# Optimization experiments

Hardware: AMD Instinct MI355X
Metric: run time of the kernel (lower is better)

## Reference

```python
import jax, jax.numpy as jnp
import numpy as np

B, S, IN, H, L = 512, 1024, 64, 32, 4


def setup_inputs() -> dict:
    key = jax.random.key(0)
    ks = jax.random.split(key, 9)
    s = 1.0 / np.sqrt(H)  # PyTorch RNN/Linear init scale
    u = lambda k, shape: jax.random.uniform(k, shape, jnp.float32, -s, s)
    return {
        "x": jax.random.normal(ks[0], (B, S, IN), jnp.float32),
        "h_state": jnp.zeros((L, B, H), jnp.float32),
        "W_ih0": u(ks[1], (H, IN)),          # layer 0 input weights
        "W_ih_rest": u(ks[2], (L - 1, H, H)),  # layers 1..3 input weights
        "W_hh": u(ks[3], (L, H, H)),
        "b_ih": u(ks[4], (L, H)),
        "b_hh": u(ks[5], (L, H)),
        "fc_w": u(ks[6], (1, H)),
        "fc_b": u(ks[7], (1,)),
    }


def _rnn_layer(seq_sbf, h0, W_ih, W_hh, b):
    # seq_sbf: [S, B, F]; vanilla RNN: h_t = tanh(x_t W_ih^T + h_{t-1} W_hh^T + b)
    def step(h, x_t):
        h = jnp.tanh(x_t @ W_ih.T + h @ W_hh.T + b)
        return h, h
    return jax.lax.scan(step, h0, seq_sbf)


def reference(x, h_state, W_ih0, W_ih_rest, W_hh, b_ih, b_hh, fc_w, fc_b):
    seq = jnp.swapaxes(x, 0, 1)  # [S, B, IN]
    h_finals = []
    for l in range(L):  # fixed small layer count
        W_ih = W_ih0 if l == 0 else W_ih_rest[l - 1]
        h_last, seq = _rnn_layer(seq, h_state[l], W_ih, W_hh[l], b_ih[l] + b_hh[l])
        h_finals.append(h_last)
    r_out = jnp.swapaxes(seq, 0, 1)                 # [B, S, H]
    logits = (r_out @ fc_w.T + fc_b)[..., 0]        # fused per-timestep Linear -> [B, S]
    probs = jax.nn.softmax(logits, axis=-1)         # nn.Softmax over last (seq) dim
    return probs, jnp.stack(h_finals, axis=0)       # [B,S], [L,B,H]
```

## Files before the change

### kernel.cpp

```cpp
#include <hip/hip_runtime.h>


#define BB 512
#define SS 1024
#define INF 64
#define HH 32
#define LL 4
#define KB 16

typedef __fp16 v2h __attribute__((ext_vector_type(2)));

__device__ __forceinline__ v2h bch(unsigned u) { return __builtin_bit_cast(v2h, u); }
__device__ __forceinline__ unsigned bcu(v2h h) { return __builtin_bit_cast(unsigned, h); }

template <int CTRL>
__device__ __forceinline__ float dpp_add(float v) {
  int y = __builtin_amdgcn_update_dpp(0, __float_as_int(v), CTRL, 0xF, 0xF, true);
  return v + __int_as_float(y);
}
template <int CTRL>
__device__ __forceinline__ float dpp_mov(float v) {
  int y = __builtin_amdgcn_update_dpp(0, __float_as_int(v), CTRL, 0xF, 0xF, true);
  return __int_as_float(y);
}

__device__ __forceinline__ float tanh_fast(float a) {
  const float e = __builtin_amdgcn_exp2f(a * 2.885390081777927f);
  const float r = __builtin_amdgcn_rcpf(e + 1.0f);
  return __builtin_fmaf(-2.0f, r, 1.0f);
}

__device__ __forceinline__ float dot16p(const v2h* w, const v2h* v) {
  float a = 0.f, c = 0.f;
#pragma unroll
  for (int j = 0; j < 4; ++j) {
    a = __builtin_amdgcn_fdot2(w[2 * j + 0], v[2 * j + 0], a, false);
    c = __builtin_amdgcn_fdot2(w[2 * j + 1], v[2 * j + 1], c, false);
  }
  return a + c;
}

#define BAR() asm volatile("s_waitcnt lgkmcnt(0)\n\ts_barrier" ::: "memory")

__global__ __launch_bounds__(512, 4) void rnn_kernel(
    const float* __restrict__ x, const float* __restrict__ h_state,
    const float* __restrict__ W_ih0, const float* __restrict__ W_ih_rest,
    const float* __restrict__ W_hh, const float* __restrict__ b_ih,
    const float* __restrict__ b_hh, const float* __restrict__ fc_w,
    const float* __restrict__ fc_b, float* __restrict__ out) {
  __shared__ int hb[LL][2][KB][16];
  __shared__ float h3f[2][KB][32];
  __shared__ float lu0[2][KB][32];
  __shared__ float lrow[SS];
  __shared__ float red[8];

  const int tid  = threadIdx.x;
  const int wid  = tid >> 6;
  const int lane = tid & 63;
  const int b    = blockIdx.x;
  const int ks   = lane & 1;
  const int h    = lane >> 1;

  v2h wih[8], whh[8];
  float bias = 0.f;
  if (wid < LL) {
    const float2* ph = (const float2*)(W_hh + (size_t)(wid * HH + h) * HH + ks * 16);
#pragma unroll
    for (int j = 0; j < 8; ++j) whh[j] = __builtin_amdgcn_cvt_pkrtz(ph[j].x, ph[j].y);
    if (wid > 0) {
      const float2* pi =
          (const float2*)(W_ih_rest + (size_t)((wid - 1) * HH + h) * HH + ks * 16);
#pragma unroll
      for (int j = 0; j < 8; ++j) wih[j] = __builtin_amdgcn_cvt_pkrtz(pi[j].x, pi[j].y);
      bias = b_ih[wid * HH + h] + b_hh[wid * HH + h];
    }
  }
  float4 wv4[8];
  float bias0 = 0.f;
  if (wid >= LL) {
    const float4* wr = (const float4*)(W_ih0 + (size_t)h * INF + ks * 32);
#pragma unroll
    for (int j = 0; j < 8; ++j) wv4[j] = wr[j];
    bias0 = b_ih[h] + b_hh[h];
  }
  const float fcwh = fc_w[h] * 0.5f;
  const float fcb  = fc_b[0];

  v2h sv[8];
  if (wid < LL) {
    const float2* hs = (const float2*)(h_state + (size_t)(wid * BB + b) * HH);
#pragma unroll
    for (int j = 0; j < 8; ++j)
      sv[j] = __builtin_amdgcn_cvt_pkrtz(hs[ks * 8 + j].x, hs[ks * 8 + j].y);
  }

  float* const hfin = out + (size_t)BB * SS;

  auto ld8 = [&](const int* p, v2h* v) __attribute__((always_inline)) {
    const uint4* q = (const uint4*)p;
    uint4 A = q[0], B = q[1];
    v[0] = bch(A.x); v[1] = bch(A.y); v[2] = bch(A.z); v[3] = bch(A.w);
    v[4] = bch(B.x); v[5] = bch(B.y); v[6] = bch(B.z); v[7] = bch(B.w);
  };
  auto packpair = [&](float hv) __attribute__((always_inline)) {
    return bcu(__builtin_amdgcn_cvt_pkrtz(hv, dpp_mov<0xEE>(hv)));
  };
  auto store_pk = [&](int l, int buf, int slot, unsigned pk) __attribute__((always_inline)) {
    if ((lane & 3) == 0) hb[l][buf][slot][lane >> 2] = (int)pk;
  };
  auto fcred = [&](float v) __attribute__((always_inline)) {
    v = dpp_add<0x111>(v);
    v = dpp_add<0x112>(v);
    v = dpp_add<0x114>(v);
    v = dpp_add<0x118>(v);
    v = dpp_add<0x142>(v);
    v = dpp_add<0x143>(v);
    return v;
  };

  if (wid == 0) {
    for (int n = 0; n < 68; ++n) {
      BAR();
      const int buf = n & 1;
      const bool fc_on = (n >= 4);
      const bool cw    = (n <= 63);
      float a[KB];
      if (fc_on) {
#pragma unroll
        for (int i = 0; i < KB; ++i) a[i] = h3f[buf ^ 1][i][h];
      }
      if (cw) {
        float ur[KB];
#pragma unroll
        for (int i = 0; i < KB; ++i) ur[i] = lu0[buf][i][h];
        float hvL = 0.f;
#pragma unroll
        for (int i = 0; i < KB; ++i) {
          float acc = dot16p(whh, sv);
          acc = dpp_add<0xB1>(acc) + ur[i];
          const float hv = tanh_fast(acc);
          const unsigned pk = packpair(hv);
          store_pk(0, buf, i, pk);
          ld8(&hb[0][buf][i][ks * 8], sv);
          if (i == KB - 1) hvL = hv;
        }
        if (n == 63 && ks == 0) hfin[(0 * BB + b) * HH + h] = hvL;
      }
      if (fc_on) {
        const int tf0 = KB * (n - 4);
#pragma unroll
        for (int i = 0; i < KB; ++i) {
          float v = fcred(a[i] * fcwh);
          if (lane == 63) lrow[tf0 + i] = v + fcb;
        }
      }
    }
  } else if (wid < LL) {
    v2h viA[4][8], viB[4][8];
    auto ldgrp = [&](int buf, int g, v2h (*vv)[8]) __attribute__((always_inline)) {
#pragma unroll
      for (int q = 0; q < 4; ++q)
        ld8(&hb[wid - 1][buf ^ 1][g * 4 + q][ks * 8], vv[q]);
    };
    auto dogrp = [&](int n, int buf, int g, v2h (*vc)[8], float& hvL)
        __attribute__((always_inline)) {
#pragma unroll
      for (int q = 0; q < 4; ++q) {
        const int i = g * 4 + q;
        float accA = dot16p(wih, vc[q]);
        float acc = accA + dot16p(whh, sv);
        acc = dpp_add<0xB1>(acc) + bias;
        const float hv = tanh_fast(acc);
        const unsigned pk = packpair(hv);
        store_pk(wid, buf, i, pk);
        if (wid == 3 && ks == 0) h3f[buf][i][h] = hv;
        ld8(&hb[wid][buf][i][ks * 8], sv);
        if (i == KB - 1) hvL = hv;
      }
    };
    auto iterl = [&](int n, int buf) __attribute__((always_inline)) {
      BAR();
      const bool cw = (n >= wid && n <= 63 + wid);
      if (cw) {
        float hvL = 0.f;
        ldgrp(buf, 0, viA);
        ldgrp(buf, 1, viB);
        dogrp(n, buf, 0, viA, hvL);
        ldgrp(buf, 2, viA);
        dogrp(n, buf, 1, viB, hvL);
        ldgrp(buf, 3, viB);
        dogrp(n, buf, 2, viA, hvL);
        dogrp(n, buf, 3, viB, hvL);
        if (n == 63 + wid && ks == 0) hfin[(wid * BB + b) * HH + h] = hvL;
      }
    };
    for (int n0 = 0; n0 < 68; n0 += 2) {
      iterl(n0, 0);
      iterl(n0 + 1, 1);
    }
  } else {
    const int p = wid - LL;
    const float* xb = x + (size_t)b * SS * INF;
    auto produce = [&](int blk) __attribute__((always_inline)) {
      const int buf = blk & 1;
      const int T = KB * blk + 4 * p;
#pragma unroll
      for (int q = 0; q < 4; ++q) {
        const float4* x4 = (const float4*)(xb + (size_t)(T + q) * INF + ks * 32);
        float acc = 0.f;
#pragma unroll
        for (int j = 0; j < 8; ++j) {
          const float4 xv = x4[j];
          acc += wv4[j].x * xv.x + wv4[j].y * xv.y + wv4[j].z * xv.z + wv4[j].w * xv.w;
        }
        const float tot = dpp_add<0xB1>(acc) + bias0;
        if (ks == 0) lu0[buf][4 * p + q][h] = tot;
      }
    };
    produce(0);
    for (int n = 0; n < 68; ++n) {
      BAR();
      if (n <= 62) produce(n + 1);
    }
  }

  __syncthreads();
  float4 v; float m; float e0, e1, e2, e3; float s;
  if (tid < 256) {
    v = ((const float4*)lrow)[tid];
    m = fmaxf(fmaxf(v.x, v.y), fmaxf(v.z, v.w));
#pragma unroll
    for (int d = 32; d >= 1; d >>= 1) m = fmaxf(m, __shfl_xor(m, d));
    if ((tid & 63) == 0) red[tid >> 6] = m;
  }
  __syncthreads();
  if (tid < 256) {
    m = fmaxf(fmaxf(red[0], red[1]), fmaxf(red[2], red[3]));
    e0 = __expf(v.x - m); e1 = __expf(v.y - m);
    e2 = __expf(v.z - m); e3 = __expf(v.w - m);
    s = (e0 + e1) + (e2 + e3);
#pragma unroll
    for (int d = 32; d >= 1; d >>= 1) s += __shfl_xor(s, d);
    if ((tid & 63) == 0) red[4 + (tid >> 6)] = s;
  }
  __syncthreads();
  if (tid < 256) {
    s = (red[4] + red[5]) + (red[6] + red[7]);
    const float inv = 1.0f / s;
    float4 o;
    o.x = e0 * inv; o.y = e1 * inv; o.z = e2 * inv; o.w = e3 * inv;
    ((float4*)(out + (size_t)b * SS))[tid] = o;
  }
}

extern "C" void kernel_launch(void* const* d_in, const int* in_sizes, int n_in,
                              void* d_out, int out_size, void* d_ws, size_t ws_size,
                              hipStream_t stream) {
  const float* x         = (const float*)d_in[0];
  const float* h_state   = (const float*)d_in[1];
  const float* W_ih0     = (const float*)d_in[2];
  const float* W_ih_rest = (const float*)d_in[3];
  const float* W_hh      = (const float*)d_in[4];
  const float* b_ih      = (const float*)d_in[5];
  const float* b_hh      = (const float*)d_in[6];
  const float* fc_w      = (const float*)d_in[7];
  const float* fc_b      = (const float*)d_in[8];
  float* out = (float*)d_out;

  hipLaunchKernelGGL(rnn_kernel, dim3(BB), dim3(512), 0, stream,
                     x, h_state, W_ih0, W_ih_rest, W_hh, b_ih, b_hh,
                     fc_w, fc_b, out);
}
```

Before: 411.1 us.

## Fold layer-0 input projection into layer waves, shrink block to four waves

Drops the four dedicated producer waves that computed the layer-0 input projection x·W_ih0. Waves 1-3 now compute those 16 timestep projections themselves, interleaved after each recurrence step, and the block shrinks from 512 to 256 threads with launch bounds adjusted. The aim is to halve threads per block so more blocks fit per CU and barrier cost drops. In exchange, the x loads and FMAs now sit on the critical path of the layer waves and raise their register pressure.

```diff
diff --git a/kernel.cpp b/kernel.cpp
--- a/kernel.cpp
+++ b/kernel.cpp
@@ -42,7 +42,7 @@
 
 #define BAR() asm volatile("s_waitcnt lgkmcnt(0)\n\ts_barrier" ::: "memory")
 
-__global__ __launch_bounds__(512, 4) void rnn_kernel(
+__global__ __launch_bounds__(256, 2) void rnn_kernel(
     const float* __restrict__ x, const float* __restrict__ h_state,
     const float* __restrict__ W_ih0, const float* __restrict__ W_ih_rest,
     const float* __restrict__ W_hh, const float* __restrict__ b_ih,
@@ -62,38 +62,39 @@
   const int h    = lane >> 1;
 
   v2h wih[8], whh[8];
+  {
+    const float2* ph = (const float2*)(W_hh + (size_t)(wid * HH + h) * HH + ks * 16);
+#pragma unroll
+    for (int j = 0; j < 8; ++j) whh[j] = __builtin_amdgcn_cvt_pkrtz(ph[j].x, ph[j].y);
+  }
   float bias = 0.f;
-  if (wid < LL) {
-    const float2* ph = (const float2*)(W_hh + (size_t)(wid * HH + h) * HH + ks * 16);
-#pragma unroll
-    for (int j = 0; j < 8; ++j) whh[j] = __builtin_amdgcn_cvt_pkrtz(ph[j].x, ph[j].y);
-    if (wid > 0) {
-      const float2* pi =
-          (const float2*)(W_ih_rest + (size_t)((wid - 1) * HH + h) * HH + ks * 16);
-#pragma unroll
-      for (int j = 0; j < 8; ++j) wih[j] = __builtin_amdgcn_cvt_pkrtz(pi[j].x, pi[j].y);
-      bias = b_ih[wid * HH + h] + b_hh[wid * HH + h];
-    }
+  if (wid > 0) {
+    const float2* pi =
+        (const float2*)(W_ih_rest + (size_t)((wid - 1) * HH + h) * HH + ks * 16);
+#pragma unroll
+    for (int j = 0; j < 8; ++j) wih[j] = __builtin_amdgcn_cvt_pkrtz(pi[j].x, pi[j].y);
   }
   float4 wv4[8];
   float bias0 = 0.f;
-  if (wid >= LL) {
+  if (wid > 0) {
     const float4* wr = (const float4*)(W_ih0 + (size_t)h * INF + ks * 32);
 #pragma unroll
     for (int j = 0; j < 8; ++j) wv4[j] = wr[j];
     bias0 = b_ih[h] + b_hh[h];
+    bias = b_ih[wid * HH + h] + b_hh[wid * HH + h];
   }
   const float fcwh = fc_w[h] * 0.5f;
   const float fcb  = fc_b[0];
 
   v2h sv[8];
-  if (wid < LL) {
+  {
     const float2* hs = (const float2*)(h_state + (size_t)(wid * BB + b) * HH);
 #pragma unroll
     for (int j = 0; j < 8; ++j)
       sv[j] = __builtin_amdgcn_cvt_pkrtz(hs[ks * 8 + j].x, hs[ks * 8 + j].y);
   }
 
+  const float* xb = x + (size_t)b * SS * INF;
   float* const hfin = out + (size_t)BB * SS;
 
   auto ld8 = [&](const int* p, v2h* v) __attribute__((always_inline)) {
@@ -116,6 +117,25 @@
     v = dpp_add<0x142>(v);
     v = dpp_add<0x143>(v);
     return v;
+  };
+  auto produce = [&](int blk) __attribute__((always_inline)) {
+    const int buf = blk & 1;
+    const int T = KB * blk;
+#pragma unroll
+    for (int q = 0; q < 6; ++q) {
+      const int i = (wid - 1) + 3 * q;
+      if (i < KB) {
+        const float4* x4 = (const float4*)(xb + (size_t)(T + i) * INF + ks * 32);
+        float acc = 0.f;
+#pragma unroll
+        for (int j = 0; j < 8; ++j) {
+          const float4 xv = x4[j];
+          acc += wv4[j].x * xv.x + wv4[j].y * xv.y + wv4[j].z * xv.z + wv4[j].w * xv.w;
+        }
+        const float tot = dpp_add<0xB1>(acc) + bias0;
+        if (ks == 0) lu0[buf][i][h] = tot;
+      }
+    }
   };
 
   if (wid == 0) {
@@ -155,7 +175,7 @@
         }
       }
     }
-  } else if (wid < LL) {
+  } else {
     v2h viA[4][8], viB[4][8];
     auto ldgrp = [&](int buf, int g, v2h (*vv)[8]) __attribute__((always_inline)) {
 #pragma unroll
@@ -178,6 +198,7 @@
         if (i == KB - 1) hvL = hv;
       }
     };
+    produce(0);
     auto iterl = [&](int n, int buf) __attribute__((always_inline)) {
       BAR();
       const bool cw = (n >= wid && n <= 63 + wid);
@@ -193,58 +214,30 @@
         dogrp(n, buf, 3, viB, hvL);
         if (n == 63 + wid && ks == 0) hfin[(wid * BB + b) * HH + h] = hvL;
       }
+      if (n <= 62) produce(n + 1);
     };
     for (int n0 = 0; n0 < 68; n0 += 2) {
       iterl(n0, 0);
       iterl(n0 + 1, 1);
     }
-  } else {
-    const int p = wid - LL;
-    const float* xb = x + (size_t)b * SS * INF;
-    auto produce = [&](int blk) __attribute__((always_inline)) {
-      const int buf = blk & 1;
-      const int T = KB * blk + 4 * p;
-#pragma unroll
-      for (int q = 0; q < 4; ++q) {
-        const float4* x4 = (const float4*)(xb + (size_t)(T + q) * INF + ks * 32);
-        float acc = 0.f;
-#pragma unroll
-        for (int j = 0; j < 8; ++j) {
-          const float4 xv = x4[j];
-          acc += wv4[j].x * xv.x + wv4[j].y * xv.y + wv4[j].z * xv.z + wv4[j].w * xv.w;
-        }
-        const float tot = dpp_add<0xB1>(acc) + bias0;
-        if (ks == 0) lu0[buf][4 * p + q][h] = tot;
-      }
-    };
-    produce(0);
-    for (int n = 0; n < 68; ++n) {
-      BAR();
-      if (n <= 62) produce(n + 1);
-    }
   }
 
   __syncthreads();
-  float4 v; float m; float e0, e1, e2, e3; float s;
-  if (tid < 256) {
-    v = ((const float4*)lrow)[tid];
-    m = fmaxf(fmaxf(v.x, v.y), fmaxf(v.z, v.w));
+  {
+    float4 v = ((const float4*)lrow)[tid];
+    float m = fmaxf(fmaxf(v.x, v.y), fmaxf(v.z, v.w));
 #pragma unroll
     for (int d = 32; d >= 1; d >>= 1) m = fmaxf(m, __shfl_xor(m, d));
     if ((tid & 63) == 0) red[tid >> 6] = m;
-  }
-  __syncthreads();
-  if (tid < 256) {
+    __syncthreads();
     m = fmaxf(fmaxf(red[0], red[1]), fmaxf(red[2], red[3]));
-    e0 = __expf(v.x - m); e1 = __expf(v.y - m);
-    e2 = __expf(v.z - m); e3 = __expf(v.w - m);
-    s = (e0 + e1) + (e2 + e3);
+    const float e0 = __expf(v.x - m), e1 = __expf(v.y - m);
+    const float e2 = __expf(v.z - m), e3 = __expf(v.w - m);
+    float s = (e0 + e1) + (e2 + e3);
 #pragma unroll
     for (int d = 32; d >= 1; d >>= 1) s += __shfl_xor(s, d);
     if ((tid & 63) == 0) red[4 + (tid >> 6)] = s;
-  }
-  __syncthreads();
-  if (tid < 256) {
+    __syncthreads();
     s = (red[4] + red[5]) + (red[6] + red[7]);
     const float inv = 1.0f / s;
     float4 o;
@@ -267,7 +260,7 @@
   const float* fc_b      = (const float*)d_in[8];
   float* out = (float*)d_out;
 
-  hipLaunchKernelGGL(rnn_kernel, dim3(BB), dim3(512), 0, stream,
+  hipLaunchKernelGGL(rnn_kernel, dim3(BB), dim3(256), 0, stream,
                      x, h_state, W_ih0, W_ih_rest, W_hh, b_ih, b_hh,
                      fc_w, fc_b, out);
 }
```

Result: slower. 555.3 us (+35.1%).
